# Kernel tuning notes

Hardware: AMD Instinct MI355X
Metric: run time of the kernel (lower is better)

Reference implementation:

```python
import jax, jax.numpy as jnp
import numpy as np

B, S, N, FI = 16, 96, 128, 1
H_LSTM, NLAYERS = 128, 3
COMB = H_LSTM + 16 * N  # 128 + 16*128 = 2176


def setup_inputs() -> dict:
    key = jax.random.key(0)
    ks = list(jax.random.split(key, 24))
    def nrm(k, shape, scale=0.1):
        return jax.random.normal(k, shape, dtype=jnp.float32) * scale
    x = jax.random.normal(ks[0], (B, S, N, FI), dtype=jnp.float32)
    adj = jax.random.randint(ks[1], (N, N), 0, 2).astype(jnp.float32)
    adj = jnp.maximum(adj, jnp.eye(N, dtype=jnp.float32))  # self-loops so no row fully masked
    return {
        "x": x, "adj": adj,
        "W_emb": nrm(ks[2], (1, 32)), "b_emb": jnp.zeros((32,), jnp.float32),
        "W1": nrm(ks[3], (32, 32)), "a1": nrm(ks[4], (64,)),
        "W2": nrm(ks[5], (32, 16)), "a2": nrm(ks[6], (32,)),
        "lstm_Wih": nrm(ks[7], (NLAYERS, 4 * H_LSTM, N)),
        "lstm_Whh": nrm(ks[8], (NLAYERS, 4 * H_LSTM, H_LSTM)),
        "lstm_bih": jnp.zeros((NLAYERS, 4 * H_LSTM), jnp.float32),
        "lstm_bhh": jnp.zeros((NLAYERS, 4 * H_LSTM), jnp.float32),
        "head_W1": nrm(ks[9], (3, COMB, 64), 0.05), "head_b1": jnp.zeros((3, 64), jnp.float32),
        "head_W2": nrm(ks[10], (3, 64, 32)), "head_b2": jnp.zeros((3, 32), jnp.float32),
        "W3d": nrm(ks[11], (32, 1)), "b3d": jnp.zeros((1,), jnp.float32),
        "W3r": nrm(ks[12], (32, 1)), "b3r": jnp.zeros((1,), jnp.float32),
        "W3v": nrm(ks[13], (32, 2)), "b3v": jnp.zeros((2,), jnp.float32),
    }


def gat(h, adj, W, a, apply_elu):
    # h: [M, N, Fin]; equivalent to concat-matmul score: e_ij = leakyrelu(a_l.Wh_i + a_r.Wh_j)
    Wh = h @ W                      # [M, N, Fout]
    f = W.shape[1]
    left = Wh @ a[:f]               # [M, N]
    right = Wh @ a[f:]              # [M, N]
    e = jax.nn.leaky_relu(left[:, :, None] + right[:, None, :], 0.2)  # [M, N, N]
    e = jnp.where(adj[None, :, :] > 0, e, jnp.float32(-9e15))
    attn = jax.nn.softmax(e, axis=2)
    out = jnp.einsum('mij,mjf->mif', attn, Wh)
    return (jax.nn.elu(out) if apply_elu else out), attn


def _lstm_layer(seq, Wih, Whh, bih, bhh):
    # seq: [B, S, D]; PyTorch gate order i, f, g, o
    Bz, Hh = seq.shape[0], Whh.shape[1]
    b = bih + bhh
    def step(carry, xt):
        h, c = carry
        g = xt @ Wih.T + h @ Whh.T + b  # [B, 4H]
        i, f, gg, o = jnp.split(g, 4, axis=1)
        c = jax.nn.sigmoid(f) * c + jax.nn.sigmoid(i) * jnp.tanh(gg)
        h = jax.nn.sigmoid(o) * jnp.tanh(c)
        return (h, c), h
    init = (jnp.zeros((Bz, Hh), seq.dtype), jnp.zeros((Bz, Hh), seq.dtype))
    _, hs = jax.lax.scan(step, init, jnp.swapaxes(seq, 0, 1))
    return jnp.swapaxes(hs, 0, 1)


def lstm_forward(seq, Wih, Whh, bih, bhh):
    h = seq
    for l in range(Wih.shape[0]):  # 3 layers (inference: inter-layer dropout is identity)
        h = _lstm_layer(h, Wih[l], Whh[l], bih[l], bhh[l])
    return h


def reference(x, adj, W_emb, b_emb, W1, a1, W2, a2,
              lstm_Wih, lstm_Whh, lstm_bih, lstm_bhh,
              head_W1, head_b1, head_W2, head_b2,
              W3d, b3d, W3r, b3r, W3v, b3v):
    Bz, Sz, Nz, _ = x.shape
    x_emb = (x @ W_emb + b_emb).reshape(Bz * Sz, Nz, -1)  # [B*S, N, 32]
    xg, _ = gat(x_emb, adj, W1, a1, True)
    xg, attn2 = gat(xg, adj, W2, a2, False)
    xg_out = xg.reshape(Bz, Sz, -1)[:, -1, :]             # [B, 16*N]
    xl = lstm_forward(x.reshape(Bz, Sz, Nz), lstm_Wih, lstm_Whh, lstm_bih, lstm_bhh)
    xl_out = xl[:, -1, :]                                 # [B, 128]
    c = jnp.concatenate([xl_out, xg_out], axis=1)         # [B, COMB]
    h1 = jax.nn.relu(jnp.einsum('bc,kcd->kbd', c, head_W1) + head_b1[:, None, :])
    h2 = jax.nn.relu(jnp.einsum('kbd,kde->kbe', h1, head_W2) + head_b2[:, None, :])
    d = h2[0] @ W3d + b3d
    r = h2[1] @ W3r + b3r
    v = h2[2] @ W3v + b3v
    return (d, r, v, attn2)
```

## Files before the change

### kernel.cpp

```cpp
#include <hip/hip_runtime.h>
#include <hip/hip_bf16.h>


typedef _Float16 half8 __attribute__((ext_vector_type(8)));
typedef float floatx4 __attribute__((ext_vector_type(4)));
typedef float float4v __attribute__((ext_vector_type(4)));

#define LOG2E 1.44269504088896f

__device__ __forceinline__ float fast_exp(float x) {
    return __builtin_amdgcn_exp2f(x * LOG2E);
}
__device__ __forceinline__ float sigm(float x) {
    x = fminf(fmaxf(x, -30.f), 30.f);
    return __builtin_amdgcn_rcpf(1.f + __builtin_amdgcn_exp2f(-x * LOG2E));
}
__device__ __forceinline__ float tanhp(float x) {
    x = fminf(fmaxf(x, -15.f), 15.f);
    float e = __builtin_amdgcn_exp2f(-2.f * LOG2E * x);
    return (1.f - e) * __builtin_amdgcn_rcpf(1.f + e);
}
__device__ __forceinline__ void split8v(float4v v0, float4v v1, half8& hi, half8& lo) {
#pragma unroll
    for (int j = 0; j < 4; ++j) {
        _Float16 h = (_Float16)v0[j];
        hi[j] = h; lo[j] = (_Float16)(v0[j] - (float)h);
    }
#pragma unroll
    for (int j = 0; j < 4; ++j) {
        _Float16 h = (_Float16)v1[j];
        hi[4 + j] = h; lo[4 + j] = (_Float16)(v1[j] - (float)h);
    }
}

struct LstmSh {
    float hbuf[2][544];
    float stage_in[16 * 132];
    float stage_out[16 * 132];
    float PreL[16 * 516];
};
struct GatSh {
    unsigned long long adjm[256];
    float xv[128];
    float u1[32], v1[32], coef[4];
    float s1v[128];
    float h2s[128 * 33];
    float wh2[128 * 17];
    float Lv[128], Rv[128], rd2[128];
    float d_h[4][128], s_h[4][128];
};
union ShU { LstmSh l; GatSh g; };

__device__ __forceinline__ void lstm_layer_body(LstmSh& sh, int b, int layer,
    const float* __restrict__ x,
    const float* __restrict__ Wih,
    const float* __restrict__ Whh,
    const float* __restrict__ bih,
    const float* __restrict__ bhh,
    float* __restrict__ Pre0,
    const float* __restrict__ HseqIn,
    float* __restrict__ HseqOut,
    int* __restrict__ fIn,
    int* __restrict__ fOut,
    float* __restrict__ xl_out)
{
    int tid = threadIdx.x;
    int w = tid >> 6, lane = tid & 63, quad = lane >> 4, sub = lane & 15;
    int hu = 16 * w + sub;
    int c4 = quad;
    const float* WihL = Wih + layer * 65536;
    const float* WhhL = Whh + layer * 65536;

    __builtin_amdgcn_s_setprio(1);

    if (layer == 0) {
        {
            half8 bhi[4][4], blo[4][4];
            float bias[4];
#pragma unroll
            for (int tt = 0; tt < 4; ++tt) {
                int r = tt * 128 + 16 * w + sub;
                bias[tt] = bih[r] + bhh[r];
#pragma unroll
                for (int kc = 0; kc < 4; ++kc) {
                    const float4v* p = (const float4v*)(WihL + r * 128 + kc * 32 + quad * 8);
                    split8v(p[0], p[1], bhi[tt][kc], blo[tt][kc]);
                }
            }
            for (int mt = 0; mt < 6; ++mt) {
                half8 ahi[4], alo[4];
                const float* arow = x + b * 12288 + (mt * 16 + sub) * 128;
#pragma unroll
                for (int kc = 0; kc < 4; ++kc) {
                    const float4v* p = (const float4v*)(arow + kc * 32 + quad * 8);
                    split8v(p[0], p[1], ahi[kc], alo[kc]);
                }
                floatx4 acc[4];
#pragma unroll
                for (int tt = 0; tt < 4; ++tt) {
                    floatx4 a = {bias[tt], bias[tt], bias[tt], bias[tt]};
                    acc[tt] = a;
                }
#pragma unroll
                for (int tt = 0; tt < 4; ++tt)
#pragma unroll
                    for (int kc = 0; kc < 4; ++kc) {
                        acc[tt] = __builtin_amdgcn_mfma_f32_16x16x32_f16(ahi[kc], bhi[tt][kc], acc[tt], 0, 0, 0);
                        acc[tt] = __builtin_amdgcn_mfma_f32_16x16x32_f16(ahi[kc], blo[tt][kc], acc[tt], 0, 0, 0);
                        acc[tt] = __builtin_amdgcn_mfma_f32_16x16x32_f16(alo[kc], bhi[tt][kc], acc[tt], 0, 0, 0);
                    }
#pragma unroll
                for (int tt = 0; tt < 4; ++tt)
#pragma unroll
                    for (int reg = 0; reg < 4; ++reg)
                        Pre0[(mt * 16 + quad * 4 + reg) * 512 + tt * 128 + 16 * w + sub] = acc[tt][reg];
            }
        }
        float4v wgt[4][8];
#pragma unroll
        for (int g = 0; g < 4; ++g) {
            const float4v* p = (const float4v*)(WhhL + (g * 128 + hu) * 128 + c4 * 32);
#pragma unroll
            for (int k = 0; k < 8; ++k) wgt[g][k] = p[k];
        }
        sh.hbuf[0][c4 * 136 + hu] = 0.f;
        float cvar = 0.f;
        __syncthreads();

        for (int t = 0; t < 96; ++t) {
            int rb = t & 1, wb = rb ^ 1;
            float pre[4];
#pragma unroll
            for (int g = 0; g < 4; ++g)
                pre[g] = Pre0[t * 512 + g * 128 + hu];
            const float4v* hc = (const float4v*)(&sh.hbuf[rb][c4 * 168]);
            float4v p4[4];
#pragma unroll
            for (int g = 0; g < 4; ++g) { float4v z = {0.f,0.f,0.f,0.f}; p4[g] = z; }
#pragma unroll
            for (int k = 0; k < 8; ++k) {
                float4v hv = hc[k];
#pragma unroll
                for (int g = 0; g < 4; ++g) p4[g] += wgt[g][k] * hv;
            }
            float p[4];
#pragma unroll
            for (int g = 0; g < 4; ++g) {
                float s = p4[g].x + p4[g].y + p4[g].z + p4[g].w;
                s += __shfl_xor(s, 16, 64);
                s += __shfl_xor(s, 32, 64);
                p[g] = s + pre[g];
            }
            float c = sigm(p[1]) * cvar + sigm(p[0]) * tanhp(p[2]);
            cvar = c;
            float h = sigm(p[3]) * tanhp(c);
            sh.hbuf[wb][c4 * 136 + hu] = h;
            if (c4 == 0) sh.stage_out[(t & 15) * 132 + hu] = h;
            __syncthreads();
            if ((t & 15) == 15) {
                int k = t >> 4;
                float* outp = HseqOut + k * 2048;
#pragma unroll
                for (int u = 0; u < 4; ++u) {
                    int e = tid * 4 + u;
                    atomicExch(&outp[e], sh.stage_out[(e >> 7) * 132 + (e & 127)]);
                }
                __syncthreads();
                if (tid == 0) atomicExch(&fOut[k], 1);
            }
        }
    } else {
        float bias[4];
#pragma unroll
        for (int tt = 0; tt < 4; ++tt) {
            int r = tt * 128 + 16 * w + sub;
            bias[tt] = bih[layer * 512 + r] + bhh[layer * 512 + r];
        }
        sh.hbuf[0][c4 * 136 + hu] = 0.f;
        float cvar = 0.f;
        __syncthreads();

        for (int k = 0; k < 6; ++k) {
            if (tid == 0) {
                while (atomicAdd(&fIn[k], 0) == 0) __builtin_amdgcn_s_sleep(16);
            }
            __syncthreads();
            {
                const float* inp = HseqIn + k * 2048;
#pragma unroll
                for (int u = 0; u < 4; ++u) {
                    int e = tid * 4 + u;
                    sh.stage_in[(e >> 7) * 132 + (e & 127)] =
                        atomicAdd((float*)&inp[e], 0.f);
                }
            }
            __syncthreads();
            {
                half8 bhi[4][4], blo[4][4];
#pragma unroll
                for (int tt = 0; tt < 4; ++tt) {
                    int r = tt * 128 + 16 * w + sub;
#pragma unroll
                    for (int kc = 0; kc < 4; ++kc) {
                        const float4v* p = (const float4v*)(WihL + r * 128 + kc * 32 + quad * 8);
                        split8v(p[0], p[1], bhi[tt][kc], blo[tt][kc]);
                    }
                }
                half8 ahi[4], alo[4];
                const float* arow = &sh.stage_in[sub * 132];
#pragma unroll
                for (int kc = 0; kc < 4; ++kc) {
                    const float4v* p = (const float4v*)(arow + kc * 32 + quad * 8);
                    split8v(p[0], p[1], ahi[kc], alo[kc]);
                }
                floatx4 acc[4];
#pragma unroll
                for (int tt = 0; tt < 4; ++tt) {
                    floatx4 a = {bias[tt], bias[tt], bias[tt], bias[tt]};
                    acc[tt] = a;
                }
#pragma unroll
                for (int tt = 0; tt < 4; ++tt)
#pragma unroll
                    for (int kc = 0; kc < 4; ++kc) {
                        acc[tt] = __builtin_amdgcn_mfma_f32_16x16x32_f16(ahi[kc], bhi[tt][kc], acc[tt], 0, 0, 0);
                        acc[tt] = __builtin_amdgcn_mfma_f32_16x16x32_f16(ahi[kc], blo[tt][kc], acc[tt], 0, 0, 0);
                        acc[tt] = __builtin_amdgcn_mfma_f32_16x16x32_f16(alo[kc], bhi[tt][kc], acc[tt], 0, 0, 0);
                    }
#pragma unroll
                for (int tt = 0; tt < 4; ++tt)
#pragma unroll
                    for (int reg = 0; reg < 4; ++reg)
                        sh.PreL[(quad * 4 + reg) * 516 + tt * 128 + 16 * w + sub] = acc[tt][reg];
            }
            __syncthreads();
            float4v wgt[4][8];
#pragma unroll
            for (int g = 0; g < 4; ++g) {
                const float4v* p = (const float4v*)(WhhL + (g * 128 + hu) * 128 + c4 * 32);
#pragma unroll
                for (int kk = 0; kk < 8; ++kk) wgt[g][kk] = p[kk];
            }
            for (int tl = 0; tl < 16; ++tl) {
                int t = k * 16 + tl;
                int rb = t & 1, wb = rb ^ 1;
                float pre[4];
#pragma unroll
                for (int g = 0; g < 4; ++g)
                    pre[g] = sh.PreL[tl * 516 + g * 128 + hu];
                const float4v* hc = (const float4v*)(&sh.hbuf[rb][c4 * 168]);
                float4v p4[4];
#pragma unroll
                for (int g = 0; g < 4; ++g) { float4v z = {0.f,0.f,0.f,0.f}; p4[g] = z; }
#pragma unroll
                for (int kk = 0; kk < 8; ++kk) {
                    float4v hv = hc[kk];
#pragma unroll
                    for (int g = 0; g < 4; ++g) p4[g] += wgt[g][kk] * hv;
                }
                float p[4];
#pragma unroll
                for (int g = 0; g < 4; ++g) {
                    float s = p4[g].x + p4[g].y + p4[g].z + p4[g].w;
                    s += __shfl_xor(s, 16, 64);
                    s += __shfl_xor(s, 32, 64);
                    p[g] = s + pre[g];
                }
                float c = sigm(p[1]) * cvar + sigm(p[0]) * tanhp(p[2]);
                cvar = c;
                float h = sigm(p[3]) * tanhp(c);
                sh.hbuf[wb][c4 * 136 + hu] = h;
                if (c4 == 0) {
                    if (layer == 1) sh.stage_out[tl * 132 + hu] = h;
                    else if (t == 95) xl_out[b * 128 + hu] = h;
                }
                __syncthreads();
            }
            if (layer == 1) {
                float* outp = HseqOut + k * 2048;
#pragma unroll
                for (int u = 0; u < 4; ++u) {
                    int e = tid * 4 + u;
                    atomicExch(&outp[e], sh.stage_out[(e >> 7) * 132 + (e & 127)]);
                }
                __syncthreads();
                if (tid == 0) atomicExch(&fOut[k], 1);
            }
        }
    }
    __builtin_amdgcn_s_setprio(0);
}

__device__ __forceinline__ void gat_body(GatSh& s, int m,
    const float* __restrict__ x, const float* __restrict__ adj,
    const float* __restrict__ W_emb, const float* __restrict__ b_emb,
    const float* __restrict__ W1, const float* __restrict__ a1,
    const float* __restrict__ W2, const float* __restrict__ a2,
    float* __restrict__ attn_out, float* __restrict__ xg)
{
    int tid = threadIdx.x;

    if (tid < 128) s.xv[tid] = x[m * 128 + tid];
#pragma unroll
    for (int base = 0; base < 16384; base += 512) {
        int idx = base + tid;
        unsigned long long msk = __ballot(adj[idx] > 0.f);
        if ((tid & 63) == 0) s.adjm[idx >> 6] = msk;
    }
    if (tid < 32) {
        float su = 0.f, sv = 0.f;
        for (int kk = 0; kk < 32; ++kk) {
            float w1v = W1[kk * 32 + tid];
            su += W_emb[kk] * w1v;
            sv += b_emb[kk] * w1v;
        }
        s.u1[tid] = su; s.v1[tid] = sv;
    }
    __syncthreads();
    if (tid < 4) {
        const float* av = a1 + ((tid >= 2) ? 32 : 0);
        const float* uv = (tid & 1) ? s.v1 : s.u1;
        float sum = 0.f;
        for (int f = 0; f < 32; ++f) sum += uv[f] * av[f];
        s.coef[tid] = sum;
    }
    __syncthreads();
    float cL = s.coef[0], dL = s.coef[1], cR = s.coef[2], dR = s.coef[3];

    {
        int i = tid & 127, q = tid >> 7;
        unsigned int ms = (unsigned int)(s.adjm[(i << 1) | (q >> 1)] >> ((q & 1) * 32));
        float Li = s.xv[i] * cL + dL;
        float den = 0.f, wsum = 0.f;
        int j0 = q * 32;
#pragma unroll
        for (int jj = 0; jj < 32; ++jj) {
            if ((ms >> jj) & 1) {
                float xj = s.xv[j0 + jj];
                float e = Li + xj * cR + dR;
                e = e > 0.f ? e : 0.2f * e;
                float p = fast_exp(e);
                den += p; wsum += p * xj;
            }
        }
        s.d_h[q][i] = den; s.s_h[q][i] = wsum;
    }
    __syncthreads();
    if (tid < 128) {
        float den = 0.f, wsum = 0.f;
#pragma unroll
        for (int q = 0; q < 4; ++q) { den += s.d_h[q][tid]; wsum += s.s_h[q][tid]; }
        s.s1v[tid] = wsum / den;
    }
    __syncthreads();
#pragma unroll
    for (int e0 = 0; e0 < 4096; e0 += 512) {
        int e = e0 + tid;
        int i = e >> 5, f = e & 31;
        float v = s.s1v[i] * s.u1[f] + s.v1[f];
        s.h2s[i * 33 + f] = v > 0.f ? v : fast_exp(v) - 1.f;
    }
    __syncthreads();
    {
        int i = tid >> 2, g0 = (tid & 3) * 4;
        float accv[4] = {0.f, 0.f, 0.f, 0.f};
        for (int f = 0; f < 32; ++f) {
            float hv = s.h2s[i * 33 + f];
#pragma unroll
            for (int g = 0; g < 4; ++g) accv[g] += hv * W2[f * 16 + g0 + g];
        }
#pragma unroll
        for (int g = 0; g < 4; ++g) s.wh2[i * 17 + g0 + g] = accv[g];
    }
    __syncthreads();
    if (tid < 256) {
        int i = tid & 127, which = tid >> 7;
        const float* aa = a2 + which * 16;
        float sum = 0.f;
#pragma unroll
        for (int g = 0; g < 16; ++g) sum += s.wh2[i * 17 + g] * aa[g];
        (which ? s.Rv : s.Lv)[i] = sum;
    }
    __syncthreads();
    {
        int i = tid & 127, q = tid >> 7;
        unsigned int ms = (unsigned int)(s.adjm[(i << 1) | (q >> 1)] >> ((q & 1) * 32));
        float Li = s.Lv[i];
        float den = 0.f;
        int j0 = q * 32;
#pragma unroll
        for (int jj = 0; jj < 32; ++jj) {
            if ((ms >> jj) & 1) {
                float e = Li + s.Rv[j0 + jj];
                e = e > 0.f ? e : 0.2f * e;
                den += fast_exp(e);
            }
        }
        s.d_h[q][i] = den;
    }
    __syncthreads();
    if (tid < 128) {
        float den = 0.f;
#pragma unroll
        for (int q = 0; q < 4; ++q) den += s.d_h[q][tid];
        s.rd2[tid] = 1.0f / den;
    }
    __syncthreads();

    float* aout = attn_out + (size_t)m * 16384;
#pragma unroll
    for (int k = 0; k < 8; ++k) {
        int e0 = k * 2048 + tid * 4;
        int i = e0 >> 7, j0 = e0 & 127;
        unsigned int bits = (unsigned int)(s.adjm[(i << 1) | (j0 >> 6)] >> (j0 & 63)) & 0xFu;
        float Li = s.Lv[i], ri = s.rd2[i];
        float4v p;
#pragma unroll
        for (int u = 0; u < 4; ++u) {
            float pv = 0.f;
            if ((bits >> u) & 1) {
                float e = Li + s.Rv[j0 + u];
                e = e > 0.f ? e : 0.2f * e;
                pv = fast_exp(e) * ri;
            }
            p[u] = pv;
        }
        *(float4v*)(aout + e0) = p;
    }

    if (m % 96 == 95) {
        int b = m / 96;
        int i = tid >> 2, g0 = (tid & 3) * 4;
        unsigned long long mA = s.adjm[i << 1], mB = s.adjm[(i << 1) | 1];
        float Li = s.Lv[i], ri = s.rd2[i];
        float accv[4] = {0.f, 0.f, 0.f, 0.f};
        for (int j = 0; j < 128; ++j) {
            unsigned long long mm = (j < 64) ? mA : mB;
            if ((mm >> (j & 63)) & 1) {
                float e = Li + s.Rv[j];
                e = e > 0.f ? e : 0.2f * e;
                float p = fast_exp(e) * ri;
#pragma unroll
                for (int g = 0; g < 4; ++g) accv[g] += p * s.wh2[j * 17 + g0 + g];
            }
        }
#pragma unroll
        for (int g = 0; g < 4; ++g) xg[b * 2048 + i * 16 + g0 + g] = accv[g];
    }
}

__global__ __launch_bounds__(512, 2) void fused_kernel(
    const float* __restrict__ x, const float* __restrict__ adj,
    const float* __restrict__ W_emb, const float* __restrict__ b_emb,
    const float* __restrict__ W1, const float* __restrict__ a1,
    const float* __restrict__ W2, const float* __restrict__ a2,
    const float* __restrict__ Wih, const float* __restrict__ Whh,
    const float* __restrict__ bih, const float* __restrict__ bhh,
    float* __restrict__ Pre, float* __restrict__ Hseq,
    int* __restrict__ flags, float* __restrict__ xl_out,
    float* __restrict__ attn_out, float* __restrict__ xg)
{
    __shared__ ShU sh;
    int bb = blockIdx.x;
    if (bb < 48) {
        int layer = bb >> 4, b = bb & 15;
        float* Pre0 = Pre + b * 49152;
        const float* HseqIn = (layer >= 1) ? Hseq + ((layer - 1) * 16 + b) * 12288 : nullptr;
        float* HseqOut = (layer <= 1) ? Hseq + (layer * 16 + b) * 12288 : nullptr;
        int* fIn  = (layer >= 1) ? flags + ((layer - 1) * 16 + b) * 8 : nullptr;
        int* fOut = (layer <= 1) ? flags + (layer * 16 + b) * 8 : nullptr;
        lstm_layer_body(sh.l, b, layer, x, Wih, Whh, bih, bhh,
                        Pre0, HseqIn, HseqOut, fIn, fOut, xl_out);
    } else {
        gat_body(sh.g, bb - 48, x, adj, W_emb, b_emb, W1, a1, W2, a2, attn_out, xg);
    }
}

__global__ __launch_bounds__(256) void head_partial_kernel(
    const float* __restrict__ xl, const float* __restrict__ xg,
    const float* __restrict__ W1, float* __restrict__ hp)
{
    int k = blockIdx.x >> 4, chunk = blockIdx.x & 15;
    int d = threadIdx.x & 63, bg = threadIdx.x >> 6;
    float acc[4] = {0.f, 0.f, 0.f, 0.f};
    int c0 = chunk * 136;
    for (int cc = c0; cc < c0 + 136; ++cc) {
        float wv = W1[(k * 2176 + cc) * 64 + d];
#pragma unroll
        for (int u = 0; u < 4; ++u) {
            int b = bg * 4 + u;
            float cv = (cc < 128) ? xl[b * 128 + cc] : xg[b * 2048 + cc - 128];
            acc[u] += wv * cv;
        }
    }
#pragma unroll
    for (int u = 0; u < 4; ++u)
        hp[(((k * 16 + chunk) * 16) + bg * 4 + u) * 64 + d] = acc[u];
}

__global__ __launch_bounds__(256) void head_final_kernel(
    const float* __restrict__ hp, const float* __restrict__ b1,
    const float* __restrict__ W2, const float* __restrict__ b2,
    const float* __restrict__ W3d, const float* __restrict__ b3d,
    const float* __restrict__ W3r, const float* __restrict__ b3r,
    const float* __restrict__ W3v, const float* __restrict__ b3v,
    float* __restrict__ out)
{
    __shared__ float h1s[3 * 16 * 64];
    __shared__ float h2s[3 * 16 * 32];
    int tid = threadIdx.x;
    for (int o = tid; o < 3072; o += 256) {
        int k = o >> 10, rem = o & 1023, b = rem >> 6, d = rem & 63;
        float s = b1[k * 64 + d];
        for (int ch = 0; ch < 16; ++ch)
            s += hp[(((k * 16 + ch) * 16) + b) * 64 + d];
        h1s[o] = fmaxf(s, 0.f);
    }
    __syncthreads();
    for (int o = tid; o < 1536; o += 256) {
        int k = o >> 9, rem = o & 511, b = rem >> 5, e = rem & 31;
        float s = b2[k * 32 + e];
        for (int dd = 0; dd < 64; ++dd)
            s += h1s[(k * 16 + b) * 64 + dd] * W2[(k * 64 + dd) * 32 + e];
        h2s[o] = fmaxf(s, 0.f);
    }
    __syncthreads();
    if (tid < 64) {
        if (tid < 16) {
            int b = tid; float s = b3d[0];
            for (int e = 0; e < 32; ++e) s += h2s[b * 32 + e] * W3d[e];
            out[b] = s;
        } else if (tid < 32) {
            int b = tid - 16; float s = b3r[0];
            for (int e = 0; e < 32; ++e) s += h2s[(16 + b) * 32 + e] * W3r[e];
            out[16 + b] = s;
        } else {
            int b = (tid - 32) >> 1, j = tid & 1; float s = b3v[j];
            for (int e = 0; e < 32; ++e) s += h2s[(32 + b) * 32 + e] * W3v[e * 2 + j];
            out[32 + b * 2 + j] = s;
        }
    }
}

extern "C" void kernel_launch(void* const* d_in, const int* in_sizes, int n_in,
                              void* d_out, int out_size, void* d_ws, size_t ws_size,
                              hipStream_t stream)
{
    const float* x     = (const float*)d_in[0];
    const float* adj   = (const float*)d_in[1];
    const float* W_emb = (const float*)d_in[2];
    const float* b_emb = (const float*)d_in[3];
    const float* W1    = (const float*)d_in[4];
    const float* a1    = (const float*)d_in[5];
    const float* W2    = (const float*)d_in[6];
    const float* a2    = (const float*)d_in[7];
    const float* Wih   = (const float*)d_in[8];
    const float* Whh   = (const float*)d_in[9];
    const float* bih   = (const float*)d_in[10];
    const float* bhh   = (const float*)d_in[11];
    const float* hW1   = (const float*)d_in[12];
    const float* hb1   = (const float*)d_in[13];
    const float* hW2   = (const float*)d_in[14];
    const float* hb2   = (const float*)d_in[15];
    const float* W3d   = (const float*)d_in[16];
    const float* b3d   = (const float*)d_in[17];
    const float* W3r   = (const float*)d_in[18];
    const float* b3r   = (const float*)d_in[19];
    const float* W3v   = (const float*)d_in[20];
    const float* b3v   = (const float*)d_in[21];

    float* out = (float*)d_out;
    float* wsf = (float*)d_ws;
    float* XG    = wsf;
    float* XL    = wsf + 32768;
    float* HP    = wsf + 34816;
    int*   FLAGS = (int*)(wsf + 83968);
    float* PRE   = wsf + 84224;
    float* HSEQ  = wsf + 870656;

    hipMemsetAsync(FLAGS, 0, 32 * 8 * sizeof(int), stream);
    fused_kernel<<<1584, 512, 0, stream>>>(
        x, adj, W_emb, b_emb, W1, a1, W2, a2,
        Wih, Whh, bih, bhh, PRE, HSEQ, FLAGS, XL, out + 64, XG);
    head_partial_kernel<<<48, 256, 0, stream>>>(XL, XG, hW1, HP);
    head_final_kernel<<<1, 256, 0, stream>>>(HP, hb1, hW2, hb2, W3d, b3d, W3r, b3r, W3v, b3v, out);
}
```

Measured before the change: 375.5 us.

## Split LSTM layers 1-2 into separate projection and recurrence blocks with ring buffer

New measurement: 353.1 us. -6.0%, faster.

```diff
diff --git a/kernel.cpp b/kernel.cpp
--- a/kernel.cpp
+++ b/kernel.cpp
@@ -35,9 +35,7 @@
 
 struct LstmSh {
     float hbuf[2][544];
-    float stage_in[16 * 132];
-    float stage_out[16 * 132];
-    float PreL[16 * 516];
+    float stage[16 * 132];
 };
 struct GatSh {
     unsigned long long adjm[256];
@@ -51,97 +49,245 @@
 };
 union ShU { LstmSh l; GatSh g; };
 
-__device__ __forceinline__ void lstm_layer_body(LstmSh& sh, int b, int layer,
-    const float* __restrict__ x,
-    const float* __restrict__ Wih,
-    const float* __restrict__ Whh,
-    const float* __restrict__ bih,
+__device__ __forceinline__ void l0_body(LstmSh& sh, int b,
+    const float* __restrict__ x, const float* __restrict__ Wih,
+    const float* __restrict__ Whh, const float* __restrict__ bih,
     const float* __restrict__ bhh,
     float* __restrict__ Pre0,
-    const float* __restrict__ HseqIn,
-    float* __restrict__ HseqOut,
-    int* __restrict__ fIn,
-    int* __restrict__ fOut,
-    float* __restrict__ xl_out)
+    float* __restrict__ Hout,
+    int* __restrict__ fHout)
 {
     int tid = threadIdx.x;
     int w = tid >> 6, lane = tid & 63, quad = lane >> 4, sub = lane & 15;
-    int hu = 16 * w + sub;
-    int c4 = quad;
+    int hu = 16 * w + sub, c4 = quad;
+
+    __builtin_amdgcn_s_setprio(1);
+    {
+        half8 bhi[4][4], blo[4][4];
+        float bias[4];
+#pragma unroll
+        for (int tt = 0; tt < 4; ++tt) {
+            int r = tt * 128 + 16 * w + sub;
+            bias[tt] = bih[r] + bhh[r];
+#pragma unroll
+            for (int kc = 0; kc < 4; ++kc) {
+                const float4v* p = (const float4v*)(Wih + r * 128 + kc * 32 + quad * 8);
+                split8v(p[0], p[1], bhi[tt][kc], blo[tt][kc]);
+            }
+        }
+        for (int mt = 0; mt < 6; ++mt) {
+            half8 ahi[4], alo[4];
+            const float* arow = x + b * 12288 + (mt * 16 + sub) * 128;
+#pragma unroll
+            for (int kc = 0; kc < 4; ++kc) {
+                const float4v* p = (const float4v*)(arow + kc * 32 + quad * 8);
+                split8v(p[0], p[1], ahi[kc], alo[kc]);
+            }
+            floatx4 acc[4];
+#pragma unroll
+            for (int tt = 0; tt < 4; ++tt) {
+                floatx4 a = {bias[tt], bias[tt], bias[tt], bias[tt]};
+                acc[tt] = a;
+            }
+#pragma unroll
+            for (int tt = 0; tt < 4; ++tt)
+#pragma unroll
+                for (int kc = 0; kc < 4; ++kc) {
+                    acc[tt] = __builtin_amdgcn_mfma_f32_16x16x32_f16(ahi[kc], bhi[tt][kc], acc[tt], 0, 0, 0);
+                    acc[tt] = __builtin_amdgcn_mfma_f32_16x16x32_f16(ahi[kc], blo[tt][kc], acc[tt], 0, 0, 0);
+                    acc[tt] = __builtin_amdgcn_mfma_f32_16x16x32_f16(alo[kc], bhi[tt][kc], acc[tt], 0, 0, 0);
+                }
+#pragma unroll
+            for (int tt = 0; tt < 4; ++tt)
+#pragma unroll
+                for (int reg = 0; reg < 4; ++reg)
+                    Pre0[(mt * 16 + quad * 4 + reg) * 512 + tt * 128 + 16 * w + sub] = acc[tt][reg];
+        }
+    }
+    float4v wgt[4][8];
+#pragma unroll
+    for (int g = 0; g < 4; ++g) {
+        const float4v* p = (const float4v*)(Whh + (g * 128 + hu) * 128 + c4 * 32);
+#pragma unroll
+        for (int k = 0; k < 8; ++k) wgt[g][k] = p[k];
+    }
+    sh.hbuf[0][c4 * 136 + hu] = 0.f;
+    float cvar = 0.f;
+    __syncthreads();
+
+    for (int t = 0; t < 96; ++t) {
+        int rb = t & 1, wb = rb ^ 1;
+        float pre[4];
+#pragma unroll
+        for (int g = 0; g < 4; ++g)
+            pre[g] = Pre0[t * 512 + g * 128 + hu];
+        const float4v* hc = (const float4v*)(&sh.hbuf[rb][c4 * 168]);
+        float4v p4[4];
+#pragma unroll
+        for (int g = 0; g < 4; ++g) { float4v z = {0.f,0.f,0.f,0.f}; p4[g] = z; }
+#pragma unroll
+        for (int k = 0; k < 8; ++k) {
+            float4v hv = hc[k];
+#pragma unroll
+            for (int g = 0; g < 4; ++g) p4[g] += wgt[g][k] * hv;
+        }
+        float p[4];
+#pragma unroll
+        for (int g = 0; g < 4; ++g) {
+            float s = p4[g].x + p4[g].y + p4[g].z + p4[g].w;
+            s += __shfl_xor(s, 16, 64);
+            s += __shfl_xor(s, 32, 64);
+            p[g] = s + pre[g];
+        }
+        float c = sigm(p[1]) * cvar + sigm(p[0]) * tanhp(p[2]);
+        cvar = c;
+        float h = sigm(p[3]) * tanhp(c);
+        sh.hbuf[wb][c4 * 136 + hu] = h;
+        if (c4 == 0) sh.stage[(t & 15) * 132 + hu] = h;
+        __syncthreads();
+        if ((t & 15) == 15) {
+            int k = t >> 4;
+            float* outp = Hout + k * 2048;
+#pragma unroll
+            for (int u = 0; u < 4; ++u) {
+                int e = tid * 4 + u;
+                atomicExch(&outp[e], sh.stage[(e >> 7) * 132 + (e & 127)]);
+            }
+            __syncthreads();
+            if (tid == 0) atomicExch(&fHout[k], 1);
+        }
+    }
+    __builtin_amdgcn_s_setprio(0);
+}
+
+__device__ __forceinline__ void proj_body(LstmSh& sh, int layer,
+    const float* __restrict__ Wih, const float* __restrict__ bih,
+    const float* __restrict__ bhh,
+    const float* __restrict__ Hin,
+    int* __restrict__ fH,
+    float* __restrict__ PreRing,
+    int* __restrict__ fP,
+    int* __restrict__ cons)
+{
+    int tid = threadIdx.x;
+    int w = tid >> 6, lane = tid & 63, quad = lane >> 4, sub = lane & 15;
     const float* WihL = Wih + layer * 65536;
+
+    half8 bhi[4][4], blo[4][4];
+    float bias[4];
+#pragma unroll
+    for (int tt = 0; tt < 4; ++tt) {
+        int r = tt * 128 + 16 * w + sub;
+        bias[tt] = bih[layer * 512 + r] + bhh[layer * 512 + r];
+#pragma unroll
+        for (int kc = 0; kc < 4; ++kc) {
+            const float4v* p = (const float4v*)(WihL + r * 128 + kc * 32 + quad * 8);
+            split8v(p[0], p[1], bhi[tt][kc], blo[tt][kc]);
+        }
+    }
+    for (int k = 0; k < 6; ++k) {
+        if (tid == 0) {
+            while (atomicAdd(&fH[k], 0) == 0) __builtin_amdgcn_s_sleep(16);
+        }
+        __syncthreads();
+        {
+            const float* inp = Hin + k * 2048;
+#pragma unroll
+            for (int u = 0; u < 4; ++u) {
+                int e = tid * 4 + u;
+                sh.stage[(e >> 7) * 132 + (e & 127)] =
+                    atomicAdd((float*)&inp[e], 0.f);
+            }
+        }
+        __syncthreads();
+        half8 ahi[4], alo[4];
+        const float* arow = &sh.stage[sub * 132];
+#pragma unroll
+        for (int kc = 0; kc < 4; ++kc) {
+            const float4v* p = (const float4v*)(arow + kc * 32 + quad * 8);
+            split8v(p[0], p[1], ahi[kc], alo[kc]);
+        }
+        floatx4 acc[4];
+#pragma unroll
+        for (int tt = 0; tt < 4; ++tt) {
+            floatx4 a = {bias[tt], bias[tt], bias[tt], bias[tt]};
+            acc[tt] = a;
+        }
+#pragma unroll
+        for (int tt = 0; tt < 4; ++tt)
+#pragma unroll
+            for (int kc = 0; kc < 4; ++kc) {
+                acc[tt] = __builtin_amdgcn_mfma_f32_16x16x32_f16(ahi[kc], bhi[tt][kc], acc[tt], 0, 0, 0);
+                acc[tt] = __builtin_amdgcn_mfma_f32_16x16x32_f16(ahi[kc], blo[tt][kc], acc[tt], 0, 0, 0);
+                acc[tt] = __builtin_amdgcn_mfma_f32_16x16x32_f16(alo[kc], bhi[tt][kc], acc[tt], 0, 0, 0);
+            }
+        if (k >= 3) {
+            if (tid == 0) {
+                while (atomicAdd(cons, 0) < k - 2) __builtin_amdgcn_s_sleep(16);
+            }
+            __syncthreads();
+        }
+        float* dst = PreRing + (k % 3) * 8192;
+#pragma unroll
+        for (int tt = 0; tt < 4; ++tt)
+#pragma unroll
+            for (int reg = 0; reg < 4; ++reg)
+                dst[(quad * 4 + reg) * 512 + tt * 128 + 16 * w + sub] = acc[tt][reg];
+        __syncthreads();
+        if (tid == 0) {
+            __threadfence();
+            atomicExch(&fP[k], 1);
+        }
+    }
+}
+
+__device__ __forceinline__ void rec_body(LstmSh& sh, int b, int layer,
+    const float* __restrict__ Whh,
+    const float* __restrict__ PreRing, int* __restrict__ fP,
+    int* __restrict__ cons,
+    float* __restrict__ Hout, int* __restrict__ fHout,
+    float* __restrict__ xl_out)
+{
+    int tid = threadIdx.x;
+    int w = tid >> 6, lane = tid & 63, quad = lane >> 4, sub = lane & 15;
+    int hu = 16 * w + sub, c4 = quad;
     const float* WhhL = Whh + layer * 65536;
 
     __builtin_amdgcn_s_setprio(1);
-
-    if (layer == 0) {
-        {
-            half8 bhi[4][4], blo[4][4];
-            float bias[4];
-#pragma unroll
-            for (int tt = 0; tt < 4; ++tt) {
-                int r = tt * 128 + 16 * w + sub;
-                bias[tt] = bih[r] + bhh[r];
-#pragma unroll
-                for (int kc = 0; kc < 4; ++kc) {
-                    const float4v* p = (const float4v*)(WihL + r * 128 + kc * 32 + quad * 8);
-                    split8v(p[0], p[1], bhi[tt][kc], blo[tt][kc]);
-                }
-            }
-            for (int mt = 0; mt < 6; ++mt) {
-                half8 ahi[4], alo[4];
-                const float* arow = x + b * 12288 + (mt * 16 + sub) * 128;
-#pragma unroll
-                for (int kc = 0; kc < 4; ++kc) {
-                    const float4v* p = (const float4v*)(arow + kc * 32 + quad * 8);
-                    split8v(p[0], p[1], ahi[kc], alo[kc]);
-                }
-                floatx4 acc[4];
-#pragma unroll
-                for (int tt = 0; tt < 4; ++tt) {
-                    floatx4 a = {bias[tt], bias[tt], bias[tt], bias[tt]};
-                    acc[tt] = a;
-                }
-#pragma unroll
-                for (int tt = 0; tt < 4; ++tt)
-#pragma unroll
-                    for (int kc = 0; kc < 4; ++kc) {
-                        acc[tt] = __builtin_amdgcn_mfma_f32_16x16x32_f16(ahi[kc], bhi[tt][kc], acc[tt], 0, 0, 0);
-                        acc[tt] = __builtin_amdgcn_mfma_f32_16x16x32_f16(ahi[kc], blo[tt][kc], acc[tt], 0, 0, 0);
-                        acc[tt] = __builtin_amdgcn_mfma_f32_16x16x32_f16(alo[kc], bhi[tt][kc], acc[tt], 0, 0, 0);
-                    }
-#pragma unroll
-                for (int tt = 0; tt < 4; ++tt)
-#pragma unroll
-                    for (int reg = 0; reg < 4; ++reg)
-                        Pre0[(mt * 16 + quad * 4 + reg) * 512 + tt * 128 + 16 * w + sub] = acc[tt][reg];
-            }
-        }
-        float4v wgt[4][8];
-#pragma unroll
-        for (int g = 0; g < 4; ++g) {
-            const float4v* p = (const float4v*)(WhhL + (g * 128 + hu) * 128 + c4 * 32);
-#pragma unroll
-            for (int k = 0; k < 8; ++k) wgt[g][k] = p[k];
-        }
-        sh.hbuf[0][c4 * 136 + hu] = 0.f;
-        float cvar = 0.f;
+    float4v wgt[4][8];
+#pragma unroll
+    for (int g = 0; g < 4; ++g) {
+        const float4v* p = (const float4v*)(WhhL + (g * 128 + hu) * 128 + c4 * 32);
+#pragma unroll
+        for (int k = 0; k < 8; ++k) wgt[g][k] = p[k];
+    }
+    sh.hbuf[0][c4 * 136 + hu] = 0.f;
+    float cvar = 0.f;
+    __syncthreads();
+
+    for (int k = 0; k < 6; ++k) {
+        if (tid == 0) {
+            while (atomicAdd(&fP[k], 0) == 0) __builtin_amdgcn_s_sleep(16);
+            __threadfence();
+        }
         __syncthreads();
-
-        for (int t = 0; t < 96; ++t) {
+        const float* PreC = PreRing + (k % 3) * 8192;
+        for (int tl = 0; tl < 16; ++tl) {
+            int t = k * 16 + tl;
             int rb = t & 1, wb = rb ^ 1;
             float pre[4];
 #pragma unroll
             for (int g = 0; g < 4; ++g)
-                pre[g] = Pre0[t * 512 + g * 128 + hu];
+                pre[g] = PreC[tl * 512 + g * 128 + hu];
             const float4v* hc = (const float4v*)(&sh.hbuf[rb][c4 * 168]);
             float4v p4[4];
 #pragma unroll
             for (int g = 0; g < 4; ++g) { float4v z = {0.f,0.f,0.f,0.f}; p4[g] = z; }
 #pragma unroll
-            for (int k = 0; k < 8; ++k) {
-                float4v hv = hc[k];
-#pragma unroll
-                for (int g = 0; g < 4; ++g) p4[g] += wgt[g][k] * hv;
+            for (int kk = 0; kk < 8; ++kk) {
+                float4v hv = hc[kk];
+#pragma unroll
+                for (int g = 0; g < 4; ++g) p4[g] += wgt[g][kk] * hv;
             }
             float p[4];
 #pragma unroll
@@ -155,137 +301,22 @@
             cvar = c;
             float h = sigm(p[3]) * tanhp(c);
             sh.hbuf[wb][c4 * 136 + hu] = h;
-            if (c4 == 0) sh.stage_out[(t & 15) * 132 + hu] = h;
+            if (c4 == 0) {
+                if (layer == 1) sh.stage[tl * 132 + hu] = h;
+                else if (t == 95) xl_out[b * 128 + hu] = h;
+            }
             __syncthreads();
-            if ((t & 15) == 15) {
-                int k = t >> 4;
-                float* outp = HseqOut + k * 2048;
-#pragma unroll
-                for (int u = 0; u < 4; ++u) {
-                    int e = tid * 4 + u;
-                    atomicExch(&outp[e], sh.stage_out[(e >> 7) * 132 + (e & 127)]);
-                }
-                __syncthreads();
-                if (tid == 0) atomicExch(&fOut[k], 1);
-            }
-        }
-    } else {
-        float bias[4];
-#pragma unroll
-        for (int tt = 0; tt < 4; ++tt) {
-            int r = tt * 128 + 16 * w + sub;
-            bias[tt] = bih[layer * 512 + r] + bhh[layer * 512 + r];
-        }
-        sh.hbuf[0][c4 * 136 + hu] = 0.f;
-        float cvar = 0.f;
-        __syncthreads();
-
-        for (int k = 0; k < 6; ++k) {
-            if (tid == 0) {
-                while (atomicAdd(&fIn[k], 0) == 0) __builtin_amdgcn_s_sleep(16);
+        }
+        if (tid == 0) atomicExch(cons, k + 1);
+        if (layer == 1) {
+            float* outp = Hout + k * 2048;
+#pragma unroll
+            for (int u = 0; u < 4; ++u) {
+                int e = tid * 4 + u;
+                atomicExch(&outp[e], sh.stage[(e >> 7) * 132 + (e & 127)]);
             }
             __syncthreads();
-            {
-                const float* inp = HseqIn + k * 2048;
-#pragma unroll
-                for (int u = 0; u < 4; ++u) {
-                    int e = tid * 4 + u;
-                    sh.stage_in[(e >> 7) * 132 + (e & 127)] =
-                        atomicAdd((float*)&inp[e], 0.f);
-                }
-            }
-            __syncthreads();
-            {
-                half8 bhi[4][4], blo[4][4];
-#pragma unroll
-                for (int tt = 0; tt < 4; ++tt) {
-                    int r = tt * 128 + 16 * w + sub;
-#pragma unroll
-                    for (int kc = 0; kc < 4; ++kc) {
-                        const float4v* p = (const float4v*)(WihL + r * 128 + kc * 32 + quad * 8);
-                        split8v(p[0], p[1], bhi[tt][kc], blo[tt][kc]);
-                    }
-                }
-                half8 ahi[4], alo[4];
-                const float* arow = &sh.stage_in[sub * 132];
-#pragma unroll
-                for (int kc = 0; kc < 4; ++kc) {
-                    const float4v* p = (const float4v*)(arow + kc * 32 + quad * 8);
-                    split8v(p[0], p[1], ahi[kc], alo[kc]);
-                }
-                floatx4 acc[4];
-#pragma unroll
-                for (int tt = 0; tt < 4; ++tt) {
-                    floatx4 a = {bias[tt], bias[tt], bias[tt], bias[tt]};
-                    acc[tt] = a;
-                }
-#pragma unroll
-                for (int tt = 0; tt < 4; ++tt)
-#pragma unroll
-                    for (int kc = 0; kc < 4; ++kc) {
-                        acc[tt] = __builtin_amdgcn_mfma_f32_16x16x32_f16(ahi[kc], bhi[tt][kc], acc[tt], 0, 0, 0);
-                        acc[tt] = __builtin_amdgcn_mfma_f32_16x16x32_f16(ahi[kc], blo[tt][kc], acc[tt], 0, 0, 0);
-                        acc[tt] = __builtin_amdgcn_mfma_f32_16x16x32_f16(alo[kc], bhi[tt][kc], acc[tt], 0, 0, 0);
-                    }
-#pragma unroll
-                for (int tt = 0; tt < 4; ++tt)
-#pragma unroll
-                    for (int reg = 0; reg < 4; ++reg)
-                        sh.PreL[(quad * 4 + reg) * 516 + tt * 128 + 16 * w + sub] = acc[tt][reg];
-            }
-            __syncthreads();
-            float4v wgt[4][8];
-#pragma unroll
-            for (int g = 0; g < 4; ++g) {
-                const float4v* p = (const float4v*)(WhhL + (g * 128 + hu) * 128 + c4 * 32);
-#pragma unroll
-                for (int kk = 0; kk < 8; ++kk) wgt[g][kk] = p[kk];
-            }
-            for (int tl = 0; tl < 16; ++tl) {
-                int t = k * 16 + tl;
-                int rb = t & 1, wb = rb ^ 1;
-                float pre[4];
-#pragma unroll
-                for (int g = 0; g < 4; ++g)
-                    pre[g] = sh.PreL[tl * 516 + g * 128 + hu];
-                const float4v* hc = (const float4v*)(&sh.hbuf[rb][c4 * 168]);
-                float4v p4[4];
-#pragma unroll
-                for (int g = 0; g < 4; ++g) { float4v z = {0.f,0.f,0.f,0.f}; p4[g] = z; }
-#pragma unroll
-                for (int kk = 0; kk < 8; ++kk) {
-                    float4v hv = hc[kk];
-#pragma unroll
-                    for (int g = 0; g < 4; ++g) p4[g] += wgt[g][kk] * hv;
-                }
-                float p[4];
-#pragma unroll
-                for (int g = 0; g < 4; ++g) {
-                    float s = p4[g].x + p4[g].y + p4[g].z + p4[g].w;
-                    s += __shfl_xor(s, 16, 64);
-                    s += __shfl_xor(s, 32, 64);
-                    p[g] = s + pre[g];
-                }
-                float c = sigm(p[1]) * cvar + sigm(p[0]) * tanhp(p[2]);
-                cvar = c;
-                float h = sigm(p[3]) * tanhp(c);
-                sh.hbuf[wb][c4 * 136 + hu] = h;
-                if (c4 == 0) {
-                    if (layer == 1) sh.stage_out[tl * 132 + hu] = h;
-                    else if (t == 95) xl_out[b * 128 + hu] = h;
-                }
-                __syncthreads();
-            }
-            if (layer == 1) {
-                float* outp = HseqOut + k * 2048;
-#pragma unroll
-                for (int u = 0; u < 4; ++u) {
-                    int e = tid * 4 + u;
-                    atomicExch(&outp[e], sh.stage_out[(e >> 7) * 132 + (e & 127)]);
-                }
-                __syncthreads();
-                if (tid == 0) atomicExch(&fOut[k], 1);
-            }
+            if (tid == 0) atomicExch(&fHout[k], 1);
         }
     }
     __builtin_amdgcn_s_setprio(0);
@@ -456,23 +487,36 @@
     const float* __restrict__ W2, const float* __restrict__ a2,
     const float* __restrict__ Wih, const float* __restrict__ Whh,
     const float* __restrict__ bih, const float* __restrict__ bhh,
-    float* __restrict__ Pre, float* __restrict__ Hseq,
+    float* __restrict__ Pre0, float* __restrict__ Pre1, float* __restrict__ Pre2,
+    float* __restrict__ H0, float* __restrict__ H1,
     int* __restrict__ flags, float* __restrict__ xl_out,
     float* __restrict__ attn_out, float* __restrict__ xg)
 {
     __shared__ ShU sh;
     int bb = blockIdx.x;
-    if (bb < 48) {
-        int layer = bb >> 4, b = bb & 15;
-        float* Pre0 = Pre + b * 49152;
-        const float* HseqIn = (layer >= 1) ? Hseq + ((layer - 1) * 16 + b) * 12288 : nullptr;
-        float* HseqOut = (layer <= 1) ? Hseq + (layer * 16 + b) * 12288 : nullptr;
-        int* fIn  = (layer >= 1) ? flags + ((layer - 1) * 16 + b) * 8 : nullptr;
-        int* fOut = (layer <= 1) ? flags + (layer * 16 + b) * 8 : nullptr;
-        lstm_layer_body(sh.l, b, layer, x, Wih, Whh, bih, bhh,
-                        Pre0, HseqIn, HseqOut, fIn, fOut, xl_out);
+    if (bb < 80) {
+        int grp = bb >> 4, b = bb & 15;
+        int* F = flags + b * 32;
+        if (grp == 0) {
+            l0_body(sh.l, b, x, Wih, Whh, bih, bhh,
+                    Pre0 + b * 49152, H0 + b * 12288, F + 0);
+        } else if (grp == 1) {
+            proj_body(sh.l, 1, Wih, bih, bhh,
+                      H0 + b * 12288, F + 0, Pre1 + b * 24576, F + 8, F + 14);
+        } else if (grp == 2) {
+            rec_body(sh.l, b, 1, Whh,
+                     Pre1 + b * 24576, F + 8, F + 14,
+                     H1 + b * 12288, F + 16, nullptr);
+        } else if (grp == 3) {
+            proj_body(sh.l, 2, Wih, bih, bhh,
+                      H1 + b * 12288, F + 16, Pre2 + b * 24576, F + 24, F + 30);
+        } else {
+            rec_body(sh.l, b, 2, Whh,
+                     Pre2 + b * 24576, F + 24, F + 30,
+                     nullptr, nullptr, xl_out);
+        }
     } else {
-        gat_body(sh.g, bb - 48, x, adj, W_emb, b_emb, W1, a1, W2, a2, attn_out, xg);
+        gat_body(sh.g, bb - 80, x, adj, W_emb, b_emb, W1, a1, W2, a2, attn_out, xg);
     }
 }
 
@@ -575,13 +619,16 @@
     float* XL    = wsf + 32768;
     float* HP    = wsf + 34816;
     int*   FLAGS = (int*)(wsf + 83968);
-    float* PRE   = wsf + 84224;
-    float* HSEQ  = wsf + 870656;
-
-    hipMemsetAsync(FLAGS, 0, 32 * 8 * sizeof(int), stream);
-    fused_kernel<<<1584, 512, 0, stream>>>(
+    float* PRE0  = wsf + 84992;
+    float* PRE1  = wsf + 871424;
+    float* PRE2  = wsf + 1264640;
+    float* H0    = wsf + 1657856;
+    float* H1    = wsf + 1854464;
+
+    hipMemsetAsync(FLAGS, 0, 16 * 32 * sizeof(int), stream);
+    fused_kernel<<<1616, 512, 0, stream>>>(
         x, adj, W_emb, b_emb, W1, a1, W2, a2,
-        Wih, Whh, bih, bhh, PRE, HSEQ, FLAGS, XL, out + 64, XG);
+        Wih, Whh, bih, bhh, PRE0, PRE1, PRE2, H0, H1, FLAGS, XL, out + 64, XG);
     head_partial_kernel<<<48, 256, 0, stream>>>(XL, XG, hW1, HP);
     head_final_kernel<<<1, 256, 0, stream>>>(HP, hb1, hW2, hb2, W3d, b3d, W3r, b3r, W3v, b3v, out);
 }
```
